# Performance work log

Hardware: AMD Instinct MI355X
Metric: run time of the kernel (lower is better)

Reference implementation:

```python
import jax, jax.numpy as jnp
import numpy as np

N, STATE_DIM, HID, D_EMB, K = 8192, 512, 128, 128, 10
EPS = 0.001


def setup_inputs() -> dict:
    key = jax.random.key(0)
    ks = jax.random.split(key, 5)
    sc = lambda fan_in: 1.0 / np.sqrt(fan_in)
    return {
        "s": jax.random.normal(ks[0], (N, STATE_DIM), dtype=jnp.float32),
        "W1": jax.random.normal(ks[1], (HID, STATE_DIM), dtype=jnp.float32) * sc(STATE_DIM),
        "b1": jax.random.normal(ks[2], (HID,), dtype=jnp.float32) * sc(STATE_DIM),
        "W2": jax.random.normal(ks[3], (D_EMB, HID), dtype=jnp.float32) * sc(HID),
        "b2": jax.random.normal(ks[4], (D_EMB,), dtype=jnp.float32) * sc(HID),
        "k": K,
    }


def reference(s, W1, b1, W2, b2, k):
    # embedding: relu(Linear) -> Linear
    x = jax.nn.relu(s @ W1.T + b1) @ W2.T + b2            # [N, d_emb]
    # pairwise L2 distance matrix: ||xi||^2 + ||xj||^2 - 2 xi.xj
    sq = jnp.sum(x * x, axis=1)                            # [N]
    dist2 = sq[:, None] + sq[None, :] - 2.0 * (x @ x.T)    # [N, N]
    # clamp tiny negative values from cancellation (torch.sqrt would NaN)
    dist = jnp.sqrt(jnp.maximum(dist2, 1e-12))             # [N, N]
    # k nearest per row, excluding self (smallest entry = own distance ~0)
    neg_vals, _ = jax.lax.top_k(-dist, k + 1)              # [N, k+1], ascending dist
    k_nearest = -neg_vals[:, 1:]                           # [N, k]
    sum_k_nearest = jnp.sum(k_nearest, axis=1, keepdims=True)  # [N, 1]
    mean_k_nearest_2 = jnp.mean(sum_k_nearest) ** 2
    return EPS / (sum_k_nearest ** 2 / mean_k_nearest_2 + EPS)
```

## Files before the change

### kernel.cpp

```cpp
#include <hip/hip_runtime.h>
#include <hip/hip_bf16.h>

#define NN 8192
#define SD 512
#define HID 128
#define DE 128
#define KP1 11
#define EPSF 0.001f
#define NSPLIT 32
#define NCHUNK NSPLIT
#define CB (NN / NSPLIT)
#define NSUB (CB / 16)
#define PBLK (8 * 2 * KP1 * 16)

using short8 = __attribute__((ext_vector_type(8))) short;
using f32x4 = __attribute__((ext_vector_type(4))) float;

__device__ inline ushort f2bf(float f) {
    __hip_bfloat16 b = __float2bfloat16(f);
    return *reinterpret_cast<ushort*>(&b);
}
__device__ inline float bf2f(ushort u) {
    unsigned v = (unsigned)u << 16;
    union { unsigned u; float f; } c; c.u = v; return c.f;
}

__global__ __launch_bounds__(256) void wsplit_kernel(
    const float* __restrict__ W1, const float* __restrict__ W2,
    ushort* __restrict__ W1h, ushort* __restrict__ W1l,
    ushort* __restrict__ W2h, ushort* __restrict__ W2l)
{
    const int bid = blockIdx.x;
    const float* src; ushort *dh, *dl; int base;
    if (bid < 64) { src = W1; dh = W1h; dl = W1l; base = bid * 1024; }
    else          { src = W2; dh = W2h; dl = W2l; base = (bid - 64) * 1024; }
    const int i = base + threadIdx.x * 4;
    float4 f = *reinterpret_cast<const float4*>(src + i);
    ushort h[4], lo[4];
    float fv[4] = {f.x, f.y, f.z, f.w};
#pragma unroll
    for (int j = 0; j < 4; ++j) {
        h[j] = f2bf(fv[j]);
        lo[j] = f2bf(fv[j] - bf2f(h[j]));
    }
    *reinterpret_cast<uint2*>(dh + i) = *reinterpret_cast<uint2*>(h);
    *reinterpret_cast<uint2*>(dl + i) = *reinterpret_cast<uint2*>(lo);
}

__global__ __launch_bounds__(512) void mlp_kernel(
    const float* __restrict__ s, const ushort* __restrict__ W1h,
    const ushort* __restrict__ W1l, const float* __restrict__ b1,
    const ushort* __restrict__ W2h, const ushort* __restrict__ W2l,
    const float* __restrict__ b2, __hip_bfloat16* __restrict__ xb,
    float* __restrict__ sqb)
{
    __shared__ __align__(16) ushort sbh[2][32 * 32];
    __shared__ __align__(16) ushort sbl[2][32 * 32];
    __shared__ __align__(16) ushort hbh[32 * 128];
    __shared__ __align__(16) ushort hbl[32 * 128];
    __shared__ __align__(16) ushort xtile[32 * 128];
    __shared__ float sqpart[8 * 32];

    const int t = threadIdx.x;
    const int w = t >> 6, l = t & 63;
    const int lc = l & 15, c4 = l >> 4;
    const int rb = blockIdx.x * 32;
    const int cb = w * 16;

    const int srow = t >> 4, sk = t & 15;
    const int ssl = ((sk >> 2) + (srow >> 2)) & 3;
    const int sByte = srow * 64 + (ssl ^ (srow & 3)) * 16 + (sk & 3) * 4;
    const float* sgbase = s + (size_t)(rb + srow) * SD + sk * 2;

    float2 sf;
#define STAGE_LOAD_S(kt_) sf = *reinterpret_cast<const float2*>(sgbase + (kt_) * 32)
#define STAGE_WRITE_S(b_) do { \
    ushort h0_ = f2bf(sf.x), h1_ = f2bf(sf.y); \
    ushort l0_ = f2bf(sf.x - bf2f(h0_)), l1_ = f2bf(sf.y - bf2f(h1_)); \
    *reinterpret_cast<unsigned*>(reinterpret_cast<char*>(sbh[b_]) + sByte) = \
        (unsigned)h0_ | ((unsigned)h1_ << 16); \
    *reinterpret_cast<unsigned*>(reinterpret_cast<char*>(sbl[b_]) + sByte) = \
        (unsigned)l0_ | ((unsigned)l1_ << 16); \
} while (0)

    int aByte[2];
#pragma unroll
    for (int rt = 0; rt < 2; ++rt) {
        int row = rt * 16 + lc;
        int sl = ((c4 + (row >> 2)) & 3) ^ (row & 3);
        aByte[rt] = row * 64 + sl * 16;
    }

    const int col = cb + lc;
    const ushort* w1hp = W1h + (size_t)col * SD + c4 * 8;
    const ushort* w1lp = W1l + (size_t)col * SD + c4 * 8;

    f32x4 acc1[2];
#pragma unroll
    for (int rt = 0; rt < 2; ++rt) acc1[rt] = {0.f, 0.f, 0.f, 0.f};

    STAGE_LOAD_S(0);
    STAGE_WRITE_S(0);
    short8 bh = *reinterpret_cast<const short8*>(w1hp);
    short8 bl = *reinterpret_cast<const short8*>(w1lp);
    short8 nbh, nbl;

    for (int kt = 0; kt < 16; ++kt) {
        __syncthreads();
        if (kt < 15) STAGE_LOAD_S(kt + 1);
        short8 ah[2], al[2];
#pragma unroll
        for (int rt = 0; rt < 2; ++rt) {
            ah[rt] = *reinterpret_cast<const short8*>(
                reinterpret_cast<char*>(sbh[kt & 1]) + aByte[rt]);
            al[rt] = *reinterpret_cast<const short8*>(
                reinterpret_cast<char*>(sbl[kt & 1]) + aByte[rt]);
        }
        if (kt < 15) {
            nbh = *reinterpret_cast<const short8*>(w1hp + (kt + 1) * 32);
            nbl = *reinterpret_cast<const short8*>(w1lp + (kt + 1) * 32);
        }
#pragma unroll
        for (int rt = 0; rt < 2; ++rt) {
            acc1[rt] = __builtin_amdgcn_mfma_f32_16x16x32_bf16(ah[rt], bh, acc1[rt], 0, 0, 0);
            acc1[rt] = __builtin_amdgcn_mfma_f32_16x16x32_bf16(ah[rt], bl, acc1[rt], 0, 0, 0);
            acc1[rt] = __builtin_amdgcn_mfma_f32_16x16x32_bf16(al[rt], bh, acc1[rt], 0, 0, 0);
        }
        if (kt < 15) {
            STAGE_WRITE_S((kt + 1) & 1);
            bh = nbh; bl = nbl;
        }
    }

    const float b1v = b1[col];
#pragma unroll
    for (int rt = 0; rt < 2; ++rt)
#pragma unroll
        for (int reg = 0; reg < 4; ++reg) {
            float v = fmaxf(acc1[rt][reg] + b1v, 0.f);
            ushort hh = f2bf(v);
            ushort hl = f2bf(v - bf2f(hh));
            int row = rt * 16 + c4 * 4 + reg;
            int sl = (col >> 3) ^ (row & 15);
            int byte = row * 256 + sl * 16 + (col & 7) * 2;
            *reinterpret_cast<ushort*>(reinterpret_cast<char*>(hbh) + byte) = hh;
            *reinterpret_cast<ushort*>(reinterpret_cast<char*>(hbl) + byte) = hl;
        }
    __syncthreads();

    f32x4 acc2[2];
#pragma unroll
    for (int rt = 0; rt < 2; ++rt) acc2[rt] = {0.f, 0.f, 0.f, 0.f};

#pragma unroll
    for (int kt = 0; kt < 4; ++kt) {
        short8 ah[2], al[2];
#pragma unroll
        for (int rt = 0; rt < 2; ++rt) {
            int row = rt * 16 + lc;
            int sl = (kt * 4 + c4) ^ (row & 15);
            int byte = row * 256 + sl * 16;
            ah[rt] = *reinterpret_cast<const short8*>(reinterpret_cast<char*>(hbh) + byte);
            al[rt] = *reinterpret_cast<const short8*>(reinterpret_cast<char*>(hbl) + byte);
        }
        short8 wh = *reinterpret_cast<const short8*>(W2h + (size_t)col * HID + kt * 32 + c4 * 8);
        short8 wl = *reinterpret_cast<const short8*>(W2l + (size_t)col * HID + kt * 32 + c4 * 8);
#pragma unroll
        for (int rt = 0; rt < 2; ++rt) {
            acc2[rt] = __builtin_amdgcn_mfma_f32_16x16x32_bf16(ah[rt], wh, acc2[rt], 0, 0, 0);
            acc2[rt] = __builtin_amdgcn_mfma_f32_16x16x32_bf16(ah[rt], wl, acc2[rt], 0, 0, 0);
            acc2[rt] = __builtin_amdgcn_mfma_f32_16x16x32_bf16(al[rt], wh, acc2[rt], 0, 0, 0);
        }
    }

    const float b2v = b2[col];
    float p[8];
#pragma unroll
    for (int j = 0; j < 8; ++j) p[j] = 0.f;
#pragma unroll
    for (int rt = 0; rt < 2; ++rt)
#pragma unroll
        for (int reg = 0; reg < 4; ++reg) {
            float v = acc2[rt][reg] + b2v;
            ushort xv = f2bf(v);
            float xf = bf2f(xv);
            p[rt * 4 + reg] = fmaf(xf, xf, p[rt * 4 + reg]);
            int row = rt * 16 + c4 * 4 + reg;
            xtile[row * 128 + col] = xv;
        }
#pragma unroll
    for (int j = 0; j < 8; ++j) {
#pragma unroll
        for (int off = 8; off >= 1; off >>= 1) p[j] += __shfl_xor(p[j], off, 16);
    }
    if (lc == 0) {
#pragma unroll
        for (int rt = 0; rt < 2; ++rt)
#pragma unroll
            for (int reg = 0; reg < 4; ++reg)
                sqpart[w * 32 + rt * 16 + c4 * 4 + reg] = p[rt * 4 + reg];
    }
    __syncthreads();
    if (t < 32) {
        float sq = 0.f;
#pragma unroll
        for (int ww = 0; ww < 8; ++ww) sq += sqpart[ww * 32 + t];
        sqb[rb + t] = sq;
    }
    const short8* xsv = reinterpret_cast<const short8*>(xtile);
    short8* xg = reinterpret_cast<short8*>(reinterpret_cast<ushort*>(xb) + (size_t)rb * DE);
    xg[t] = xsv[t];
}

__global__ __launch_bounds__(512) void knn_kernel(
    const ushort* __restrict__ xs, const float* __restrict__ sqb,
    float* __restrict__ part)
{
    __shared__ __align__(16) ushort lbuf[CB * DE];
    __shared__ __align__(16) float sqs[CB];

    const int bid = blockIdx.x;
    const int rid = bid >> 5, cid = bid & 31;
    const int t = threadIdx.x;
    const int w = t >> 6, l = t & 63;
    const int q16 = l & 15, lg = l >> 4;
    const int kk = lg * 8;
    const int qb = rid * 256 + w * 32;
    const int cstart = cid * CB;

    {
        const ushort* sb = xs + (size_t)cstart * DE;
#pragma unroll
        for (int i = 0; i < 8; ++i) {
            int sl = t + 512 * i;
            int row = sl >> 4, col = sl & 15;
            short8 v = *reinterpret_cast<const short8*>(sb + row * DE + col * 8);
            *reinterpret_cast<short8*>(&lbuf[(row * 16 + (col ^ (row & 7))) * 8]) = v;
        }
        if (t < 64)
            reinterpret_cast<float4*>(sqs)[t] =
                reinterpret_cast<const float4*>(sqb + cstart)[t];
    }

    short8 bq[2][4];
#pragma unroll
    for (int qs = 0; qs < 2; ++qs)
#pragma unroll
        for (int kb = 0; kb < 4; ++kb)
            bq[qs][kb] = *reinterpret_cast<const short8*>(
                xs + (size_t)(qb + qs * 16 + q16) * DE + kb * 32 + kk);

    float m[2][KP1];
#pragma unroll
    for (int qs = 0; qs < 2; ++qs)
#pragma unroll
        for (int j = 0; j < KP1; ++j) m[qs][j] = 1e30f;

#define INS(qs_, v_) do { \
    float d2_ = (v_); \
    _Pragma("unroll") \
    for (int j_ = KP1 - 1; j_ >= 1; --j_) \
        m[qs_][j_] = __builtin_amdgcn_fmed3f(d2_, m[qs_][j_ - 1], m[qs_][j_]); \
    m[qs_][0] = fminf(d2_, m[qs_][0]); \
} while (0)

    int aIdx[4];
#pragma unroll
    for (int kb = 0; kb < 4; ++kb)
        aIdx[kb] = (q16 * 16 + ((kb * 4 + lg) ^ (q16 & 7))) * 8;

    __syncthreads();

    for (int st = 0; st < NSUB; ++st) {
        const ushort* lb = lbuf + st * 2048;
        short8 fa[4];
#pragma unroll
        for (int kb = 0; kb < 4; ++kb)
            fa[kb] = *reinterpret_cast<const short8*>(lb + aIdx[kb]);
        float4 sv = *reinterpret_cast<const float4*>(sqs + st * 16 + lg * 4);
#pragma unroll
        for (int qs = 0; qs < 2; ++qs) {
            f32x4 acc = {0.f, 0.f, 0.f, 0.f};
#pragma unroll
            for (int kb = 0; kb < 4; ++kb)
                acc = __builtin_amdgcn_mfma_f32_16x16x32_bf16(fa[kb], bq[qs][kb], acc, 0, 0, 0);
            INS(qs, fmaf(-2.f, acc[0], sv.x));
            INS(qs, fmaf(-2.f, acc[1], sv.y));
            INS(qs, fmaf(-2.f, acc[2], sv.z));
            INS(qs, fmaf(-2.f, acc[3], sv.w));
        }
    }

    __syncthreads();
    float* mb = reinterpret_cast<float*>(lbuf);
#pragma unroll
    for (int qs = 0; qs < 2; ++qs)
#pragma unroll
        for (int j = 0; j < KP1; ++j)
            mb[(((w * 2 + qs) * 4 + lg) * KP1 + j) * 16 + q16] = m[qs][j];
    __syncthreads();
    if (l < 32) {
        const int qs = l >> 4, qq = l & 15;
        float mm[KP1];
#pragma unroll
        for (int j = 0; j < KP1; ++j)
            mm[j] = mb[(((w * 2 + qs) * 4 + 0) * KP1 + j) * 16 + qq];
#pragma unroll
        for (int g = 1; g < 4; ++g)
#pragma unroll
            for (int j = 0; j < KP1; ++j) {
                float d2 = mb[(((w * 2 + qs) * 4 + g) * KP1 + j) * 16 + qq];
#pragma unroll
                for (int jj = KP1 - 1; jj >= 1; --jj)
                    mm[jj] = __builtin_amdgcn_fmed3f(d2, mm[jj - 1], mm[jj]);
                mm[0] = fminf(d2, mm[0]);
            }
        float* pout = part + (size_t)bid * PBLK;
#pragma unroll
        for (int j = 0; j < KP1; ++j)
            pout[((w * 2 + qs) * KP1 + j) * 16 + qq] = mm[j];
    }
}

__global__ __launch_bounds__(256) void merge_kernel(
    const float* __restrict__ part, const float* __restrict__ sqb,
    float* __restrict__ sumk, float* __restrict__ psum)
{
    __shared__ float rowsum[8];
    const int t = threadIdx.x;
    const int ww = t >> 6, l = t & 63;
    const int half = l >> 5, c = l & 31;
    const int row = blockIdx.x * 8 + ww * 2 + half;
    const int rid = row >> 8;
    const int sub = (row >> 4) & 15;
    const int qq = row & 15;
    const float* pl = part + (size_t)(rid * 32 + c) * PBLK + sub * (KP1 * 16) + qq;

    float m[KP1];
#pragma unroll
    for (int j = 0; j < KP1; ++j) m[j] = pl[j * 16];

#pragma unroll
    for (int s = 1; s <= 16; s <<= 1) {
        float o[KP1];
#pragma unroll
        for (int j = 0; j < KP1; ++j) o[j] = __shfl_xor(m[j], s, 64);
#pragma unroll
        for (int j = 0; j < KP1; ++j) {
            float d2 = o[j];
#pragma unroll
            for (int jj = KP1 - 1; jj >= 1; --jj)
                m[jj] = __builtin_amdgcn_fmed3f(d2, m[jj - 1], m[jj]);
            m[0] = fminf(d2, m[0]);
        }
    }

    if (c == 0) {
        const float sqq = sqb[row];
        float sum = 0.f;
#pragma unroll
        for (int j = 1; j < KP1; ++j)
            sum += sqrtf(fmaxf(m[j] + sqq, 1e-12f));
        sumk[row] = sum;
        rowsum[ww * 2 + half] = sum;
    }
    __syncthreads();
    if (t == 0) {
        float p = 0.f;
#pragma unroll
        for (int i = 0; i < 8; ++i) p += rowsum[i];
        psum[blockIdx.x] = p;
    }
}

__global__ __launch_bounds__(256) void final_kernel(
    const float* __restrict__ sumk, const float* __restrict__ psum,
    float* __restrict__ out)
{
    __shared__ float qsh;
    __shared__ float red[4];
    const int t = threadIdx.x;
    {
        float p = 0.f;
#pragma unroll
        for (int i = 0; i < 4; ++i) p += psum[t + i * 256];
#pragma unroll
        for (int off = 32; off >= 1; off >>= 1) p += __shfl_xor(p, off, 64);
        if ((t & 63) == 0) red[t >> 6] = p;
    }
    __syncthreads();
    if (t == 0) {
        float mean = (red[0] + red[1] + red[2] + red[3]) * (1.0f / NN);
        qsh = EPSF * mean * mean;
    }
    __syncthreads();
    const float qq = qsh;
    const int i = blockIdx.x * 256 + t;
    const float sv = sumk[i];
    out[i] = qq / (fmaf(sv, sv, qq));
}

extern "C" void kernel_launch(void* const* d_in, const int* in_sizes, int n_in,
                              void* d_out, int out_size, void* d_ws, size_t ws_size,
                              hipStream_t stream)
{
    const float* s  = (const float*)d_in[0];
    const float* W1 = (const float*)d_in[1];
    const float* b1 = (const float*)d_in[2];
    const float* W2 = (const float*)d_in[3];
    const float* b2 = (const float*)d_in[4];
    float* out = (float*)d_out;

    char* ws = (char*)d_ws;
    __hip_bfloat16* xb = (__hip_bfloat16*)ws;
    float* sqb  = (float*)(ws + (size_t)NN * DE * 2);
    float* part = sqb + NN;
    float* sumk = part + (size_t)1024 * PBLK;
    float* psum = sumk + NN;
    ushort* W1h = (ushort*)(psum + 1024);
    ushort* W1l = W1h + (size_t)HID * SD;
    ushort* W2h = W1l + (size_t)HID * SD;
    ushort* W2l = W2h + (size_t)DE * HID;

    wsplit_kernel<<<80, 256, 0, stream>>>(W1, W2, W1h, W1l, W2h, W2l);
    mlp_kernel<<<NN / 32, 512, 0, stream>>>(s, W1h, W1l, b1, W2h, W2l, b2, xb, sqb);
    knn_kernel<<<(NN / 256) * NSPLIT, 512, 0, stream>>>((const ushort*)xb, sqb, part);
    merge_kernel<<<NN / 8, 256, 0, stream>>>(part, sqb, sumk, psum);
    final_kernel<<<NN / 256, 256, 0, stream>>>(sumk, psum, out);
}
```

Measured before the change: 76.42 us.

## Fuse weight splitting into MLP and merge final normalization via last-block counter

```diff
diff --git a/kernel.cpp b/kernel.cpp
--- a/kernel.cpp
+++ b/kernel.cpp
@@ -24,33 +24,21 @@
     unsigned v = (unsigned)u << 16;
     union { unsigned u; float f; } c; c.u = v; return c.f;
 }
-
-__global__ __launch_bounds__(256) void wsplit_kernel(
-    const float* __restrict__ W1, const float* __restrict__ W2,
-    ushort* __restrict__ W1h, ushort* __restrict__ W1l,
-    ushort* __restrict__ W2h, ushort* __restrict__ W2l)
-{
-    const int bid = blockIdx.x;
-    const float* src; ushort *dh, *dl; int base;
-    if (bid < 64) { src = W1; dh = W1h; dl = W1l; base = bid * 1024; }
-    else          { src = W2; dh = W2h; dl = W2l; base = (bid - 64) * 1024; }
-    const int i = base + threadIdx.x * 4;
-    float4 f = *reinterpret_cast<const float4*>(src + i);
-    ushort h[4], lo[4];
-    float fv[4] = {f.x, f.y, f.z, f.w};
-#pragma unroll
-    for (int j = 0; j < 4; ++j) {
-        h[j] = f2bf(fv[j]);
-        lo[j] = f2bf(fv[j] - bf2f(h[j]));
-    }
-    *reinterpret_cast<uint2*>(dh + i) = *reinterpret_cast<uint2*>(h);
-    *reinterpret_cast<uint2*>(dl + i) = *reinterpret_cast<uint2*>(lo);
+__device__ inline void split8(const float4 a, const float4 b, short8& hi, short8& lo) {
+    float v[8] = {a.x, a.y, a.z, a.w, b.x, b.y, b.z, b.w};
+    ushort h[8], lw[8];
+#pragma unroll
+    for (int j = 0; j < 8; ++j) {
+        h[j] = f2bf(v[j]);
+        lw[j] = f2bf(v[j] - bf2f(h[j]));
+    }
+    hi = *reinterpret_cast<short8*>(h);
+    lo = *reinterpret_cast<short8*>(lw);
 }
 
 __global__ __launch_bounds__(512) void mlp_kernel(
-    const float* __restrict__ s, const ushort* __restrict__ W1h,
-    const ushort* __restrict__ W1l, const float* __restrict__ b1,
-    const ushort* __restrict__ W2h, const ushort* __restrict__ W2l,
+    const float* __restrict__ s, const float* __restrict__ W1,
+    const float* __restrict__ b1, const float* __restrict__ W2,
     const float* __restrict__ b2, __hip_bfloat16* __restrict__ xb,
     float* __restrict__ sqb)
 {
@@ -92,8 +80,7 @@
     }
 
     const int col = cb + lc;
-    const ushort* w1hp = W1h + (size_t)col * SD + c4 * 8;
-    const ushort* w1lp = W1l + (size_t)col * SD + c4 * 8;
+    const float* w1p = W1 + (size_t)col * SD + c4 * 8;
 
     f32x4 acc1[2];
 #pragma unroll
@@ -101,9 +88,9 @@
 
     STAGE_LOAD_S(0);
     STAGE_WRITE_S(0);
-    short8 bh = *reinterpret_cast<const short8*>(w1hp);
-    short8 bl = *reinterpret_cast<const short8*>(w1lp);
-    short8 nbh, nbl;
+    float4 wf0 = *reinterpret_cast<const float4*>(w1p);
+    float4 wf1 = *reinterpret_cast<const float4*>(w1p + 4);
+    float4 nwf0, nwf1;
 
     for (int kt = 0; kt < 16; ++kt) {
         __syncthreads();
@@ -117,9 +104,11 @@
                 reinterpret_cast<char*>(sbl[kt & 1]) + aByte[rt]);
         }
         if (kt < 15) {
-            nbh = *reinterpret_cast<const short8*>(w1hp + (kt + 1) * 32);
-            nbl = *reinterpret_cast<const short8*>(w1lp + (kt + 1) * 32);
-        }
+            nwf0 = *reinterpret_cast<const float4*>(w1p + (kt + 1) * 32);
+            nwf1 = *reinterpret_cast<const float4*>(w1p + (kt + 1) * 32 + 4);
+        }
+        short8 bh, bl;
+        split8(wf0, wf1, bh, bl);
 #pragma unroll
         for (int rt = 0; rt < 2; ++rt) {
             acc1[rt] = __builtin_amdgcn_mfma_f32_16x16x32_bf16(ah[rt], bh, acc1[rt], 0, 0, 0);
@@ -128,7 +117,7 @@
         }
         if (kt < 15) {
             STAGE_WRITE_S((kt + 1) & 1);
-            bh = nbh; bl = nbl;
+            wf0 = nwf0; wf1 = nwf1;
         }
     }
 
@@ -152,6 +141,7 @@
 #pragma unroll
     for (int rt = 0; rt < 2; ++rt) acc2[rt] = {0.f, 0.f, 0.f, 0.f};
 
+    const float* w2p = W2 + (size_t)col * HID + c4 * 8;
 #pragma unroll
     for (int kt = 0; kt < 4; ++kt) {
         short8 ah[2], al[2];
@@ -163,8 +153,10 @@
             ah[rt] = *reinterpret_cast<const short8*>(reinterpret_cast<char*>(hbh) + byte);
             al[rt] = *reinterpret_cast<const short8*>(reinterpret_cast<char*>(hbl) + byte);
         }
-        short8 wh = *reinterpret_cast<const short8*>(W2h + (size_t)col * HID + kt * 32 + c4 * 8);
-        short8 wl = *reinterpret_cast<const short8*>(W2l + (size_t)col * HID + kt * 32 + c4 * 8);
+        float4 w0 = *reinterpret_cast<const float4*>(w2p + kt * 32);
+        float4 w1v = *reinterpret_cast<const float4*>(w2p + kt * 32 + 4);
+        short8 wh, wl;
+        split8(w0, w1v, wh, wl);
 #pragma unroll
         for (int rt = 0; rt < 2; ++rt) {
             acc2[rt] = __builtin_amdgcn_mfma_f32_16x16x32_bf16(ah[rt], wh, acc2[rt], 0, 0, 0);
@@ -322,11 +314,16 @@
     }
 }
 
-__global__ __launch_bounds__(256) void merge_kernel(
+__global__ __launch_bounds__(256) void merge_final_kernel(
     const float* __restrict__ part, const float* __restrict__ sqb,
-    float* __restrict__ sumk, float* __restrict__ psum)
+    float* __restrict__ sumk, float* __restrict__ psum,
+    unsigned* __restrict__ counter, float* __restrict__ out)
 {
     __shared__ float rowsum[8];
+    __shared__ unsigned done;
+    __shared__ float qsh;
+    __shared__ float red[4];
+
     const int t = threadIdx.x;
     const int ww = t >> 6, l = t & 63;
     const int half = l >> 5, c = l & 31;
@@ -371,15 +368,13 @@
         for (int i = 0; i < 8; ++i) p += rowsum[i];
         psum[blockIdx.x] = p;
     }
-}
-
-__global__ __launch_bounds__(256) void final_kernel(
-    const float* __restrict__ sumk, const float* __restrict__ psum,
-    float* __restrict__ out)
-{
-    __shared__ float qsh;
-    __shared__ float red[4];
-    const int t = threadIdx.x;
+    __threadfence();
+    __syncthreads();
+    if (t == 0) done = atomicAdd(counter, 1u);
+    __syncthreads();
+    if (done != gridDim.x - 1) return;
+
+    __threadfence();
     {
         float p = 0.f;
 #pragma unroll
@@ -394,10 +389,11 @@
         qsh = EPSF * mean * mean;
     }
     __syncthreads();
-    const float qq = qsh;
-    const int i = blockIdx.x * 256 + t;
-    const float sv = sumk[i];
-    out[i] = qq / (fmaf(sv, sv, qq));
+    const float qv = qsh;
+    for (int i = t; i < NN; i += 256) {
+        const float sv = sumk[i];
+        out[i] = qv / (fmaf(sv, sv, qv));
+    }
 }
 
 extern "C" void kernel_launch(void* const* d_in, const int* in_sizes, int n_in,
@@ -417,14 +413,10 @@
     float* part = sqb + NN;
     float* sumk = part + (size_t)1024 * PBLK;
     float* psum = sumk + NN;
-    ushort* W1h = (ushort*)(psum + 1024);
-    ushort* W1l = W1h + (size_t)HID * SD;
-    ushort* W2h = W1l + (size_t)HID * SD;
-    ushort* W2l = W2h + (size_t)DE * HID;
-
-    wsplit_kernel<<<80, 256, 0, stream>>>(W1, W2, W1h, W1l, W2h, W2l);
-    mlp_kernel<<<NN / 32, 512, 0, stream>>>(s, W1h, W1l, b1, W2h, W2l, b2, xb, sqb);
+    unsigned* counter = (unsigned*)(psum + 1024);
+
+    hipMemsetAsync(counter, 0, sizeof(unsigned), stream);
+    mlp_kernel<<<NN / 32, 512, 0, stream>>>(s, W1, b1, W2, b2, xb, sqb);
     knn_kernel<<<(NN / 256) * NSPLIT, 512, 0, stream>>>((const ushort*)xb, sqb, part);
-    merge_kernel<<<NN / 8, 256, 0, stream>>>(part, sqb, sumk, psum);
-    final_kernel<<<NN / 256, 256, 0, stream>>>(sumk, psum, out);
-}
+    merge_final_kernel<<<NN / 8, 256, 0, stream>>>(part, sqb, sumk, psum, counter, out);
+}
```

New measurement: 143.3 us. 1.88x slower.
